# Kernel tuning notes

Hardware: AMD Instinct MI355X
Metric: run time of the kernel (lower is better)

The kernel has to match this reference:

```python
import jax, jax.numpy as jnp
import numpy as np

B, S, D_IN, D_OUT, R = 4, 1024, 1024, 1024, 8

def setup_inputs() -> dict:
    key = jax.random.key(0)
    k1, k2, k3, k4, k5 = jax.random.split(key, 5)
    scale = 1.0 / np.sqrt(D_IN)
    return {
        "x": jax.random.normal(k1, (B, S, D_IN), dtype=jnp.float32),
        "A_params": jax.random.normal(k2, (B, S, D_OUT, R), dtype=jnp.float32) * 0.02,
        "B_params": jax.random.normal(k3, (B, S, R, D_IN), dtype=jnp.float32) * 0.02,
        "W": jax.random.normal(k4, (D_OUT, D_IN), dtype=jnp.float32) * scale,
        "b": jax.random.normal(k5, (D_OUT,), dtype=jnp.float32) * scale,
    }

def reference(x, A_params, B_params, W, b):
    # base linear: y = x @ W^T + b  -> [B, S, D_OUT]
    base_out = jnp.einsum('bsi,oi->bso', x, W) + b
    # per-token low-rank update: (x @ B^T) @ A^T
    inter = jnp.einsum('bsi,bsri->bsr', x, B_params)           # [B, S, R]
    adaptation = jnp.einsum('bsr,bsor->bso', inter, A_params)  # [B, S, D_OUT]
    return base_out + adaptation
```

## Files before the change

### kernel.cpp

```cpp
#include <hip/hip_runtime.h>
#include <hip/hip_bf16.h>
#include <stdint.h>

#define TOKENS 4096
#define DIN 1024
#define DOUT 1024
#define RANK 8

typedef __attribute__((ext_vector_type(4))) float f32x4;
typedef __attribute__((ext_vector_type(8))) short short8;

__device__ __forceinline__ unsigned short f2bf(float f) {
    union { float f; unsigned u; } v; v.f = f;
    unsigned r = v.u + 0x7FFFu + ((v.u >> 16) & 1u);
    return (unsigned short)(r >> 16);
}

__global__ __launch_bounds__(256) void k_convert_w(const float* __restrict__ W,
                                                   ushort* __restrict__ Wb) {
    int i = blockIdx.x * 256 + threadIdx.x;
    float4 v = ((const float4*)W)[i];
    ushort4 u;
    u.x = f2bf(v.x); u.y = f2bf(v.y); u.z = f2bf(v.z); u.w = f2bf(v.w);
    ((ushort4*)Wb)[i] = u;
}

__global__ __launch_bounds__(256) void k_lora(const float* __restrict__ x,
                                              const float* __restrict__ Bp,
                                              const float* __restrict__ Ap,
                                              const float* __restrict__ bias,
                                              float* __restrict__ out,
                                              ushort* __restrict__ xb) {
    const int t = blockIdx.x;
    const int tid = threadIdx.x;
    const int lane = tid & 63, wave = tid >> 6;

    float4 xv = ((const float4*)(x + (size_t)t * DIN))[tid];

    ushort4 u;
    u.x = f2bf(xv.x); u.y = f2bf(xv.y); u.z = f2bf(xv.z); u.w = f2bf(xv.w);
    ((ushort4*)(xb + (size_t)t * DIN))[tid] = u;

    const float4* B4 = (const float4*)(Bp + (size_t)t * RANK * DIN);
    float acc[RANK];
#pragma unroll
    for (int r = 0; r < RANK; ++r) {
        float4 bv = B4[r * 256 + tid];
        acc[r] = xv.x * bv.x + xv.y * bv.y + xv.z * bv.z + xv.w * bv.w;
    }

    __shared__ float part[4][RANK];
    __shared__ float sint[RANK];
#pragma unroll
    for (int r = 0; r < RANK; ++r) {
        float v = acc[r];
#pragma unroll
        for (int off = 32; off > 0; off >>= 1) v += __shfl_xor(v, off, 64);
        if (lane == 0) part[wave][r] = v;
    }
    __syncthreads();
    if (tid < RANK)
        sint[tid] = part[0][tid] + part[1][tid] + part[2][tid] + part[3][tid];
    __syncthreads();

    const float i0 = sint[0], i1 = sint[1], i2 = sint[2], i3 = sint[3];
    const float i4 = sint[4], i5 = sint[5], i6 = sint[6], i7 = sint[7];

    const float4* A4 = (const float4*)(Ap + ((size_t)t * DOUT + tid * 4) * RANK);
    float res[4];
#pragma unroll
    for (int j = 0; j < 4; ++j) {
        float4 a0 = A4[j * 2], a1 = A4[j * 2 + 1];
        res[j] = a0.x * i0 + a0.y * i1 + a0.z * i2 + a0.w * i3 +
                 a1.x * i4 + a1.y * i5 + a1.z * i6 + a1.w * i7;
    }
    float4 bb = ((const float4*)bias)[tid];
    float4 o4;
    o4.x = res[0] + bb.x; o4.y = res[1] + bb.y;
    o4.z = res[2] + bb.z; o4.w = res[3] + bb.w;
    ((float4*)(out + (size_t)t * DOUT))[tid] = o4;
}

__global__ __launch_bounds__(256) void k_gemm_add(const ushort* __restrict__ Xb,
                                                  const ushort* __restrict__ Wb,
                                                  float* __restrict__ out) {
    __shared__ ushort As[128 * 64];
    __shared__ ushort Bs[64 * 64];

    const int tid = threadIdx.x;
    const int lane = tid & 63, wave = tid >> 6;
    const int wm = wave >> 1, wn = wave & 1;
    const int M0 = blockIdx.y * 128;
    const int N0 = blockIdx.x * 64;
    const int col16 = lane & 15;
    const int kg = lane >> 4;

    f32x4 acc[4][2] = {};

    for (int kt = 0; kt < DIN; kt += 64) {
        __syncthreads();
#pragma unroll
        for (int it = 0; it < 4; ++it) {
            int flat = it * 256 + tid;
            int row = flat >> 3, ch = flat & 7;
            const ushort* g = Xb + (size_t)(M0 + row) * DIN + kt + ch * 8;
            __builtin_amdgcn_global_load_lds(
                (const __attribute__((address_space(1))) void*)g,
                (__attribute__((address_space(3))) void*)(As + flat * 8), 16, 0, 0);
        }
#pragma unroll
        for (int it = 0; it < 2; ++it) {
            int flat = it * 256 + tid;
            int row = flat >> 3, ch = flat & 7;
            const ushort* g = Wb + (size_t)(N0 + row) * DIN + kt + ch * 8;
            __builtin_amdgcn_global_load_lds(
                (const __attribute__((address_space(1))) void*)g,
                (__attribute__((address_space(3))) void*)(Bs + flat * 8), 16, 0, 0);
        }
        asm volatile("s_waitcnt vmcnt(0)" ::: "memory");
        __syncthreads();

#pragma unroll
        for (int ks = 0; ks < 2; ++ks) {
            short8 a[4], b[2];
#pragma unroll
            for (int mf = 0; mf < 4; ++mf)
                a[mf] = *(const short8*)(As + (wm * 64 + mf * 16 + col16) * 64 + ks * 32 + kg * 8);
#pragma unroll
            for (int nf = 0; nf < 2; ++nf)
                b[nf] = *(const short8*)(Bs + (wn * 32 + nf * 16 + col16) * 64 + ks * 32 + kg * 8);
#pragma unroll
            for (int mf = 0; mf < 4; ++mf)
#pragma unroll
                for (int nf = 0; nf < 2; ++nf)
                    acc[mf][nf] = __builtin_amdgcn_mfma_f32_16x16x32_bf16(
                        a[mf], b[nf], acc[mf][nf], 0, 0, 0);
        }
    }

#pragma unroll
    for (int nf = 0; nf < 2; ++nf) {
        int o = N0 + wn * 32 + nf * 16 + col16;
#pragma unroll
        for (int mf = 0; mf < 4; ++mf) {
#pragma unroll
            for (int rg = 0; rg < 4; ++rg) {
                int m = M0 + wm * 64 + mf * 16 + kg * 4 + rg;
                size_t idx = (size_t)m * DOUT + o;
                out[idx] += acc[mf][nf][rg];
            }
        }
    }
}

extern "C" void kernel_launch(void* const* d_in, const int* in_sizes, int n_in,
                              void* d_out, int out_size, void* d_ws, size_t ws_size,
                              hipStream_t stream) {
    const float* x    = (const float*)d_in[0];
    const float* Ap   = (const float*)d_in[1];
    const float* Bp   = (const float*)d_in[2];
    const float* W    = (const float*)d_in[3];
    const float* bias = (const float*)d_in[4];
    float* out = (float*)d_out;

    ushort* xb = (ushort*)d_ws;
    ushort* Wb = xb + (size_t)TOKENS * DIN;

    hipLaunchKernelGGL(k_convert_w, dim3(DOUT * DIN / 1024), dim3(256), 0, stream, W, Wb);
    hipLaunchKernelGGL(k_lora, dim3(TOKENS), dim3(256), 0, stream,
                       x, Bp, Ap, bias, out, xb);
    hipLaunchKernelGGL(k_gemm_add, dim3(DOUT / 64, TOKENS / 128), dim3(256), 0, stream,
                       xb, Wb, out);
}
```

Before: 82.61 us.

## Fuse LoRA adaptation and bias into GEMM epilogue, removing output round-trip

The first kernel now only computes the rank-8 intermediate per token and the bf16 copy of x. The GEMM epilogue loads the per-token A_params rows, takes the dot product with the intermediate cached in shared memory, adds the bias and writes the output once. This removes the full fp32 output write plus the read-modify-write in the GEMM. The cost is that the epilogue's A_params loads are strided, with each lane reading 32 bytes at a stride of 32 bytes per column, which may coalesce less well than before.

```diff
diff --git a/kernel.cpp b/kernel.cpp
--- a/kernel.cpp
+++ b/kernel.cpp
@@ -25,12 +25,10 @@
     ((ushort4*)Wb)[i] = u;
 }
 
-__global__ __launch_bounds__(256) void k_lora(const float* __restrict__ x,
-                                              const float* __restrict__ Bp,
-                                              const float* __restrict__ Ap,
-                                              const float* __restrict__ bias,
-                                              float* __restrict__ out,
-                                              ushort* __restrict__ xb) {
+__global__ __launch_bounds__(256) void k_inter(const float* __restrict__ x,
+                                               const float* __restrict__ Bp,
+                                               float* __restrict__ inter,
+                                               ushort* __restrict__ xb) {
     const int t = blockIdx.x;
     const int tid = threadIdx.x;
     const int lane = tid & 63, wave = tid >> 6;
@@ -50,7 +48,6 @@
     }
 
     __shared__ float part[4][RANK];
-    __shared__ float sint[RANK];
 #pragma unroll
     for (int r = 0; r < RANK; ++r) {
         float v = acc[r];
@@ -60,32 +57,20 @@
     }
     __syncthreads();
     if (tid < RANK)
-        sint[tid] = part[0][tid] + part[1][tid] + part[2][tid] + part[3][tid];
-    __syncthreads();
-
-    const float i0 = sint[0], i1 = sint[1], i2 = sint[2], i3 = sint[3];
-    const float i4 = sint[4], i5 = sint[5], i6 = sint[6], i7 = sint[7];
-
-    const float4* A4 = (const float4*)(Ap + ((size_t)t * DOUT + tid * 4) * RANK);
-    float res[4];
-#pragma unroll
-    for (int j = 0; j < 4; ++j) {
-        float4 a0 = A4[j * 2], a1 = A4[j * 2 + 1];
-        res[j] = a0.x * i0 + a0.y * i1 + a0.z * i2 + a0.w * i3 +
-                 a1.x * i4 + a1.y * i5 + a1.z * i6 + a1.w * i7;
-    }
-    float4 bb = ((const float4*)bias)[tid];
-    float4 o4;
-    o4.x = res[0] + bb.x; o4.y = res[1] + bb.y;
-    o4.z = res[2] + bb.z; o4.w = res[3] + bb.w;
-    ((float4*)(out + (size_t)t * DOUT))[tid] = o4;
+        inter[(size_t)t * RANK + tid] =
+            part[0][tid] + part[1][tid] + part[2][tid] + part[3][tid];
 }
 
-__global__ __launch_bounds__(256) void k_gemm_add(const ushort* __restrict__ Xb,
-                                                  const ushort* __restrict__ Wb,
-                                                  float* __restrict__ out) {
+__global__ __launch_bounds__(256) void k_gemm_fused(const ushort* __restrict__ Xb,
+                                                    const ushort* __restrict__ Wb,
+                                                    const float* __restrict__ bias,
+                                                    const float* __restrict__ inter,
+                                                    const float* __restrict__ Ap,
+                                                    float* __restrict__ out) {
     __shared__ ushort As[128 * 64];
     __shared__ ushort Bs[64 * 64];
+    __shared__ float sInter[128 * 9];
+    __shared__ float sBias[64];
 
     const int tid = threadIdx.x;
     const int lane = tid & 63, wave = tid >> 6;
@@ -94,6 +79,13 @@
     const int N0 = blockIdx.x * 64;
     const int col16 = lane & 15;
     const int kg = lane >> 4;
+
+    {
+        float4 v = ((const float4*)(inter + (size_t)M0 * RANK))[tid];
+        float* p = sInter + (tid >> 1) * 9 + (tid & 1) * 4;
+        p[0] = v.x; p[1] = v.y; p[2] = v.z; p[3] = v.w;
+        if (tid < 16) ((float4*)sBias)[tid] = ((const float4*)(bias + N0))[tid];
+    }
 
     f32x4 acc[4][2] = {};
 
@@ -140,14 +132,21 @@
 
 #pragma unroll
     for (int nf = 0; nf < 2; ++nf) {
-        int o = N0 + wn * 32 + nf * 16 + col16;
+        const int oc = wn * 32 + nf * 16 + col16;
+        const int o = N0 + oc;
+        const float bb = sBias[oc];
 #pragma unroll
         for (int mf = 0; mf < 4; ++mf) {
 #pragma unroll
             for (int rg = 0; rg < 4; ++rg) {
-                int m = M0 + wm * 64 + mf * 16 + kg * 4 + rg;
-                size_t idx = (size_t)m * DOUT + o;
-                out[idx] += acc[mf][nf][rg];
+                const int mloc = wm * 64 + mf * 16 + kg * 4 + rg;
+                const int m = M0 + mloc;
+                const float4* A8 = (const float4*)(Ap + ((size_t)m * DOUT + o) * RANK);
+                float4 a0 = A8[0], a1 = A8[1];
+                const float* iv = sInter + mloc * 9;
+                float ad = a0.x * iv[0] + a0.y * iv[1] + a0.z * iv[2] + a0.w * iv[3] +
+                           a1.x * iv[4] + a1.y * iv[5] + a1.z * iv[6] + a1.w * iv[7];
+                out[(size_t)m * DOUT + o] = acc[mf][nf][rg] + bb + ad;
             }
         }
     }
@@ -165,10 +164,10 @@
 
     ushort* xb = (ushort*)d_ws;
     ushort* Wb = xb + (size_t)TOKENS * DIN;
+    float* inter = (float*)(Wb + (size_t)DOUT * DIN);
 
     hipLaunchKernelGGL(k_convert_w, dim3(DOUT * DIN / 1024), dim3(256), 0, stream, W, Wb);
-    hipLaunchKernelGGL(k_lora, dim3(TOKENS), dim3(256), 0, stream,
-                       x, Bp, Ap, bias, out, xb);
-    hipLaunchKernelGGL(k_gemm_add, dim3(DOUT / 64, TOKENS / 128), dim3(256), 0, stream,
-                       xb, Wb, out);
+    hipLaunchKernelGGL(k_inter, dim3(TOKENS), dim3(256), 0, stream, x, Bp, inter, xb);
+    hipLaunchKernelGGL(k_gemm_fused, dim3(DOUT / 64, TOKENS / 128), dim3(256), 0, stream,
+                       xb, Wb, bias, inter, Ap, out);
 }
```

After: 82.25 us. No clear change (-0.4%).
